# Kernel optimization log

Hardware: AMD Instinct MI355X
Metric: run time of the kernel (lower is better)

Reference implementation:

```python
import math
import jax, jax.numpy as jnp
import numpy as np

EPS = 1e-5
D_MODEL, N_HEADS, D_HEAD = 512, 8, 64


def make_signed_quant(num_bits):
    Qn = -2 ** (num_bits - 1)
    Qp = 2 ** (num_bits - 1) - 1

    @jax.custom_vjp
    def quant(x, alpha):
        a = jnp.maximum(alpha, EPS)
        return jnp.clip(jnp.round(x / a), Qn, Qp) * a

    def fwd(x, alpha):
        a = jnp.maximum(alpha, EPS)
        return jnp.clip(jnp.round(x / a), Qn, Qp) * a, (x, a)

    def bwd(res, g):
        x, a = res
        qw = x / a
        small = (qw < Qn).astype(g.dtype)
        big = (qw > Qp).astype(g.dtype)
        mid = 1.0 - small - big
        gs = 1.0 / math.sqrt(x.size * Qp)
        ga = jnp.sum((small * Qn + big * Qp + mid * (jnp.round(qw) - qw)) * g) * gs
        return mid * g, ga.reshape(())

    quant.defvjp(fwd, bwd)
    return quant


def make_unsigned_quant(num_bits):
    Qp = 2 ** num_bits - 1

    @jax.custom_vjp
    def quant(x, alpha):
        a = jnp.maximum(alpha, EPS)
        mn = jnp.min(x)
        return jnp.clip(jnp.round((x - mn) / a), 0, Qp) * a + mn

    def fwd(x, alpha):
        a = jnp.maximum(alpha, EPS)
        mn = jnp.min(x)
        return jnp.clip(jnp.round((x - mn) / a), 0, Qp) * a + mn, (x - mn, a)

    def bwd(res, g):
        xs, a = res
        qw = xs / a
        small = (qw < 0).astype(g.dtype)
        big = (qw > Qp).astype(g.dtype)
        mid = 1.0 - small - big
        gs = 1.0 / math.sqrt(xs.size * Qp)
        ga = jnp.sum((big * Qp + mid * (jnp.round(qw) - qw)) * g) * gs
        return mid * g, ga.reshape(())

    quant.defvjp(fwd, bwd)
    return quant


def _bwn_body(w):
    # layerwise BWN: sign(w - mean(w)) * mean(|w|)
    m = jnp.mean(jnp.abs(w))
    e = jnp.mean(w)
    return jnp.sign(w - e) * m


@jax.custom_vjp
def bwn(w):
    return _bwn_body(w)


def _bwn_fwd(w):
    return _bwn_body(w), None


def _bwn_bwd(_, g):
    return (g,)  # straight-through


bwn.defvjp(_bwn_fwd, _bwn_bwd)

sig4 = make_signed_quant(4)
sig8 = make_signed_quant(8)  # the output QuantizeLinear uses default input_bits=8
uns4 = make_unsigned_quant(4)


def layernorm(x, g, b):
    mu = jnp.mean(x, axis=-1, keepdims=True)
    var = jnp.var(x, axis=-1, keepdims=True)
    return (x - mu) / jnp.sqrt(var + 1e-5) * g + b


def attention_forward(q, k, v, Wq, Wk, Wv, Wo, bq, bk, bv, ln_g, ln_b,
                      aq_in, ak_in, av_in, a_cq, a_ck, a_cv, a_cattn, ao_in):
    B, S, _ = q.shape
    # QuantizeLinear: 4-bit elastic act quant + BWN binary weights, NO bias; then LearnableBias add
    Q = sig4(q, aq_in) @ bwn(Wq).T + bq
    K = sig4(k, ak_in) @ bwn(Wk).T + bk
    V = sig4(v, av_in) @ bwn(Wv).T + bv

    def split(x):  # [B,S,H*d] -> [B,H,S,d]
        return jnp.transpose(x.reshape(B, -1, N_HEADS, D_HEAD), (0, 2, 1, 3))

    Q, K, V = split(Q), split(K), split(V)
    Q = sig4(Q, a_cq)
    K = sig4(K, a_ck)
    V = sig4(V, a_cv)
    scores = jnp.einsum('bhqd,bhkd->bhqk', Q, K) / math.sqrt(D_HEAD)
    # NOTE: original calls scores.masked_fill(mask==0, -1e9) WITHOUT assignment,
    # so the mask has no effect on the math; replicated faithfully.
    attn = jax.nn.softmax(scores, axis=-1)
    attn = uns4(attn, a_cattn)
    ctx = jnp.einsum('bhqk,bhkd->bhqd', attn, V)
    # faithful to original `.view(B, S, H*d)` on the [B,H,S,d] tensor (no head transpose)
    ctx = ctx.reshape(B, S, N_HEADS * D_HEAD)
    out = sig8(ctx, ao_in) @ bwn(Wo).T
    return layernorm(q + out, ln_g, ln_b), scores


def setup_inputs() -> dict:
    key = jax.random.key(0)
    ks = jax.random.split(key, 8)
    B, S, D = 4, 1024, 512
    f = jnp.float32
    return {
        'q': jax.random.normal(ks[0], (B, S, D), f),
        'k': jax.random.normal(ks[1], (B, S, D), f),
        'v': jax.random.normal(ks[2], (B, S, D), f),
        'mask': jnp.ones((B, 1, S, S), jnp.int32),
        'Wq': jax.random.normal(ks[3], (D, D), f) * 0.02,
        'Wk': jax.random.normal(ks[4], (D, D), f) * 0.02,
        'Wv': jax.random.normal(ks[5], (D, D), f) * 0.02,
        'Wo': jax.random.normal(ks[6], (D, D), f) * 0.02,
        'bq': jnp.zeros((D,), f),
        'bk': jnp.zeros((D,), f),
        'bv': jnp.zeros((D,), f),
        'ln_g': jnp.ones((D,), f),
        'ln_b': jnp.zeros((D,), f),
        'aq_in': jnp.asarray(0.5, f),
        'ak_in': jnp.asarray(0.5, f),
        'av_in': jnp.asarray(0.5, f),
        'a_cq': jnp.asarray(0.2, f),
        'a_ck': jnp.asarray(0.2, f),
        'a_cv': jnp.asarray(0.2, f),
        'a_cattn': jnp.asarray(0.002, f),
        'ao_in': jnp.asarray(0.01, f),
    }


def reference(q, k, v, mask, Wq, Wk, Wv, Wo, bq, bk, bv, ln_g, ln_b,
              aq_in, ak_in, av_in, a_cq, a_ck, a_cv, a_cattn, ao_in):
    # mask is structurally unused (original masked_fill is not in-place and discarded)
    return attention_forward(q, k, v, Wq, Wk, Wv, Wo, bq, bk, bv, ln_g, ln_b,
                             aq_in, ak_in, av_in, a_cq, a_ck, a_cv, a_cattn, ao_in)
```

## Files before the change

kernel.cpp:

```cpp
#include <hip/hip_runtime.h>
#include <math.h>
#include <stdint.h>

#define EPSQ 1e-5f
#define WELEM 262144
#define OUT0N 2097152

#define O_WSUM   0
#define O_WABS   16
#define O_MN     32
#define O_COLSUM 64
#define O_SIGNS  16384
#define O_KQ     (O_SIGNS + 4*WELEM)
#define O_KK     (O_KQ + 2097152)
#define O_KV     (O_KK + 2097152)
#define O_VT     (O_KV + 2097152)
#define O_RMAX   (O_VT + 2097152)
#define O_RSUM   (O_RMAX + 131072)
#define O_CTXQ   (O_RSUM + 131072)
#define O_OUTB   (O_CTXQ + 2097152)
#define O_RCAND  O_OUTB

#define AS 72

typedef __bf16 bf16x8 __attribute__((ext_vector_type(8)));
typedef __bf16 bf16x4 __attribute__((ext_vector_type(4)));
typedef float  floatx4 __attribute__((ext_vector_type(4)));

__device__ __forceinline__ float clampf(float x, float lo, float hi) {
  return fminf(fmaxf(x, lo), hi);
}

__device__ __forceinline__ void unpack16(__bf16* dst, int4 raw) {
  const int8_t* sb = (const int8_t*)&raw;
  __bf16 tmp[16];
#pragma unroll
  for (int j = 0; j < 16; ++j) tmp[j] = (__bf16)(float)sb[j];
  *(bf16x8*)&dst[0] = *(bf16x8*)&tmp[0];
  *(bf16x8*)&dst[8] = *(bf16x8*)&tmp[8];
}

__global__ void k_init(float* wsum, float* wabs) {
  int t = threadIdx.x;
  if (t < 4) { wsum[t] = 0.f; wabs[t] = 0.f; }
}

__global__ void k_wstats(const float* Wq, const float* Wk, const float* Wv, const float* Wo,
                         float* wsum, float* wabs) {
  __shared__ float s1[256], s2[256];
  int w = blockIdx.x >> 6;
  const float* W = (w == 0) ? Wq : (w == 1) ? Wk : (w == 2) ? Wv : Wo;
  int base = (blockIdx.x & 63) * 4096;
  float s = 0.f, sa = 0.f;
  for (int i = threadIdx.x; i < 4096; i += 256) {
    float x = W[base + i];
    s += x; sa += fabsf(x);
  }
  s1[threadIdx.x] = s; s2[threadIdx.x] = sa; __syncthreads();
  for (int o = 128; o > 0; o >>= 1) {
    if (threadIdx.x < o) { s1[threadIdx.x] += s1[threadIdx.x + o]; s2[threadIdx.x] += s2[threadIdx.x + o]; }
    __syncthreads();
  }
  if (threadIdx.x == 0) { atomicAdd(&wsum[w], s1[0]); atomicAdd(&wabs[w], s2[0]); }
}

__global__ void k_sign(const float* Wq, const float* Wk, const float* Wv, const float* Wo,
                       const float* wsum, int8_t* signs) {
  int idx = blockIdx.x * 256 + threadIdx.x;
  int w = idx >> 18;
  int pos = idx & (WELEM - 1);
  const float* W = (w == 0) ? Wq : (w == 1) ? Wk : (w == 2) ? Wv : Wo;
  float e = wsum[w] * (1.0f / 262144.0f);
  float x = W[pos];
  signs[idx] = (int8_t)((x > e) - (x < e));
}

__global__ __launch_bounds__(256) void k_proj(
    const float* q, const float* kin, const float* vin,
    const float* bq, const float* bk, const float* bv,
    const float* aq, const float* ak, const float* av,
    const float* acq, const float* ack, const float* acv,
    const int8_t* signs, const float* wabs,
    int8_t* kqo, int8_t* kko, int8_t* kvo) {
  __shared__ __align__(16) __bf16 As[64][AS];
  __shared__ __align__(16) __bf16 Bs[64][AS];
  int z = blockIdx.z;
  const float* X    = (z == 0) ? q   : (z == 1) ? kin : vin;
  const float* bias = (z == 0) ? bq  : (z == 1) ? bk  : bv;
  const float* aip  = (z == 0) ? aq  : (z == 1) ? ak  : av;
  const float* ahp  = (z == 0) ? acq : (z == 1) ? ack : acv;
  int8_t* outp      = (z == 0) ? kqo : (z == 1) ? kko : kvo;
  float a_in = fmaxf(aip[0], EPSQ);
  float a_hd = fmaxf(ahp[0], EPSQ);
  float m_w  = wabs[z] * (1.0f / 262144.0f);
  const int8_t* S = signs + (size_t)z * WELEM;

  int n0 = blockIdx.x * 64;
  int f0 = blockIdx.y * 64;
  int t = threadIdx.x;
  int lane = t & 63, w = t >> 6, quad = lane >> 4, l16 = lane & 15;
  int c4 = (t & 15) * 4, mb = t >> 4;
  int k16 = (t & 3) * 16, mrow = t >> 2;
  floatx4 acc[4];
#pragma unroll
  for (int nt = 0; nt < 4; ++nt) acc[nt] = (floatx4){0.f, 0.f, 0.f, 0.f};

  for (int k0 = 0; k0 < 512; k0 += 64) {
#pragma unroll
    for (int j = 0; j < 4; ++j) {
      int m = mb + j * 16;
      float4 x = *(const float4*)&X[(size_t)(n0 + m) * 512 + k0 + c4];
      bf16x4 av = { (__bf16)clampf(rintf(x.x / a_in), -8.f, 7.f),
                    (__bf16)clampf(rintf(x.y / a_in), -8.f, 7.f),
                    (__bf16)clampf(rintf(x.z / a_in), -8.f, 7.f),
                    (__bf16)clampf(rintf(x.w / a_in), -8.f, 7.f) };
      *(bf16x4*)&As[m][c4] = av;
    }
    {
      int4 raw = *(const int4*)&S[(size_t)(f0 + mrow) * 512 + k0 + k16];
      unpack16(&Bs[mrow][k16], raw);
    }
    __syncthreads();
#pragma unroll
    for (int kh = 0; kh < 64; kh += 32) {
      bf16x8 a = *(const bf16x8*)&As[w * 16 + l16][kh + quad * 8];
#pragma unroll
      for (int nt = 0; nt < 4; ++nt) {
        bf16x8 b = *(const bf16x8*)&Bs[nt * 16 + l16][kh + quad * 8];
        acc[nt] = __builtin_amdgcn_mfma_f32_16x16x32_bf16(a, b, acc[nt], 0, 0, 0);
      }
    }
    __syncthreads();
  }
  float s_am = a_in * m_w;
#pragma unroll
  for (int nt = 0; nt < 4; ++nt) {
    int f = f0 + nt * 16 + l16;
    int h = f >> 6, dd = f & 63;
    float bia = bias[f];
#pragma unroll
    for (int r = 0; r < 4; ++r) {
      int n = n0 + w * 16 + quad * 4 + r;
      int b = n >> 10, srow = n & 1023;
      float P = s_am * acc[nt][r] + bia;
      float hq = clampf(rintf(P / a_hd), -8.f, 7.f);
      outp[(size_t)((b * 8 + h) * 1024 + srow) * 64 + dd] = (int8_t)hq;
    }
  }
}

__global__ __launch_bounds__(256) void k_vt(const int8_t* kv, int8_t* vt, int* colsum) {
  __shared__ int red[256];
  int bh = blockIdx.x;
  int t = threadIdx.x;
  int dd = t & 63, part = t >> 6;
  const int8_t* p = kv + (size_t)bh * 65536;
  int8_t* o = vt + (size_t)bh * 65536;
  int acc = 0;
  for (int s = part * 256; s < part * 256 + 256; ++s) {
    int8_t val = p[s * 64 + dd];
    o[dd * 1024 + s] = val;
    acc += val;
  }
  red[t] = acc; __syncthreads();
  if (part == 0) colsum[bh * 64 + dd] = red[dd] + red[64 + dd] + red[128 + dd] + red[192 + dd];
}

__global__ __launch_bounds__(256) void k_qks(
    const int8_t* kq, const int8_t* kkv,
    const float* acq, const float* ack,
    float* scores, float* rmax, float* rsum, float* rcand) {
  __shared__ __align__(16) __bf16 As[64][AS];
  __shared__ __align__(16) __bf16 Bs[64][AS];
  int bh = blockIdx.y;
  int q0 = blockIdx.x * 64;
  const int8_t* A  = kq  + (size_t)bh * 65536;
  const int8_t* Bp = kkv + (size_t)bh * 65536;
  float* Sp = scores + ((size_t)bh * 1024 + q0) * 1024;
  int t = threadIdx.x;
  int lane = t & 63, w = t >> 6, quad = lane >> 4, l16 = lane & 15;
  int k16 = (t & 3) * 16, mrow = t >> 2;
  float sc = fmaxf(acq[0], EPSQ) * fmaxf(ack[0], EPSQ) * 0.125f;

  {
    int4 ra = *(const int4*)&A[(q0 + mrow) * 64 + k16];
    unpack16(&As[mrow][k16], ra);
  }
  float m_run[4], l_run[4], mn_run[4];
#pragma unroll
  for (int rr = 0; rr < 4; ++rr) { m_run[rr] = -INFINITY; l_run[rr] = 0.f; mn_run[rr] = INFINITY; }

  for (int ct = 0; ct < 16; ++ct) {
    __syncthreads();
    {
      int4 rb = *(const int4*)&Bp[(ct * 64 + mrow) * 64 + k16];
      unpack16(&Bs[mrow][k16], rb);
    }
    __syncthreads();
    floatx4 acc[4];
#pragma unroll
    for (int nt = 0; nt < 4; ++nt) acc[nt] = (floatx4){0.f, 0.f, 0.f, 0.f};
#pragma unroll
    for (int kh = 0; kh < 64; kh += 32) {
      bf16x8 a = *(const bf16x8*)&As[w * 16 + l16][kh + quad * 8];
#pragma unroll
      for (int nt = 0; nt < 4; ++nt) {
        bf16x8 b = *(const bf16x8*)&Bs[nt * 16 + l16][kh + quad * 8];
        acc[nt] = __builtin_amdgcn_mfma_f32_16x16x32_bf16(a, b, acc[nt], 0, 0, 0);
      }
    }
#pragma unroll
    for (int rr = 0; rr < 4; ++rr) {
      int row = w * 16 + quad * 4 + rr;
      float v[4];
#pragma unroll
      for (int nt = 0; nt < 4; ++nt) {
        v[nt] = sc * acc[nt][rr];
        Sp[(size_t)row * 1024 + ct * 64 + nt * 16 + l16] = v[nt];
      }
      float tmax = fmaxf(fmaxf(v[0], v[1]), fmaxf(v[2], v[3]));
      float tmin = fminf(fminf(v[0], v[1]), fminf(v[2], v[3]));
      mn_run[rr] = fminf(mn_run[rr], tmin);
      float mnew = fmaxf(m_run[rr], tmax);
      float s = 0.f;
#pragma unroll
      for (int nt = 0; nt < 4; ++nt) s += expf(v[nt] - mnew);
      l_run[rr] = l_run[rr] * expf(m_run[rr] - mnew) + s;
      m_run[rr] = mnew;
    }
  }
#pragma unroll
  for (int o = 1; o < 16; o <<= 1) {
#pragma unroll
    for (int rr = 0; rr < 4; ++rr) {
      float mo = __shfl_xor(m_run[rr], o);
      float lo = __shfl_xor(l_run[rr], o);
      float mnew = fmaxf(m_run[rr], mo);
      l_run[rr] = l_run[rr] * expf(m_run[rr] - mnew) + lo * expf(mo - mnew);
      m_run[rr] = mnew;
      mn_run[rr] = fminf(mn_run[rr], __shfl_xor(mn_run[rr], o));
    }
  }
  if (l16 == 0) {
#pragma unroll
    for (int rr = 0; rr < 4; ++rr) {
      int r = bh * 1024 + q0 + w * 16 + quad * 4 + rr;
      rmax[r] = m_run[rr];
      rsum[r] = l_run[rr];
      rcand[r] = expf(mn_run[rr] - m_run[rr]) * (1.0f / l_run[rr]);
    }
  }
}

__global__ __launch_bounds__(1024) void k_minred(const float* rcand, float* mnf) {
  __shared__ float red[1024];
  float mn = INFINITY;
  for (int i = threadIdx.x; i < 32768; i += 1024) mn = fminf(mn, rcand[i]);
  red[threadIdx.x] = mn; __syncthreads();
  for (int o = 512; o > 0; o >>= 1) {
    if (threadIdx.x < o) red[threadIdx.x] = fminf(red[threadIdx.x], red[threadIdx.x + o]);
    __syncthreads();
  }
  if (threadIdx.x == 0) mnf[0] = red[0];
}

__global__ __launch_bounds__(256) void k_pv(
    const float* scores, const float* rmax, const float* rsum,
    const float* mnf, const int* colsum, const int8_t* vt,
    const float* acattn, const float* acv, const float* ao,
    int8_t* ctxq) {
  __shared__ __align__(16) __bf16 As[32][AS];
  __shared__ __align__(16) __bf16 Bs[64][AS];
  int bh = blockIdx.y;
  int m0 = blockIdx.x * 32;
  float mn = mnf[0];
  float a_att = fmaxf(acattn[0], EPSQ);
  float a_v   = fmaxf(acv[0], EPSQ);
  float a_o   = fmaxf(ao[0], EPSQ);
  const float* Sp  = scores + (size_t)bh * 1048576;
  const int8_t* Vt = vt + (size_t)bh * 65536;
  int t = threadIdx.x;
  int lane = t & 63, w = t >> 6, quad = lane >> 4, l16 = lane & 15;
  int mt = w & 1, np = w >> 1;
  int c4 = (t & 15) * 4, mb = t >> 4;
  int k16 = (t & 3) * 16, mrow = t >> 2;
  float rm[2], rs[2];
#pragma unroll
  for (int j = 0; j < 2; ++j) {
    int r = bh * 1024 + m0 + mb + j * 16;
    rm[j] = rmax[r]; rs[j] = rsum[r];
  }
  floatx4 acc[2];
  acc[0] = (floatx4){0.f, 0.f, 0.f, 0.f};
  acc[1] = (floatx4){0.f, 0.f, 0.f, 0.f};

  for (int k0 = 0; k0 < 1024; k0 += 64) {
#pragma unroll
    for (int j = 0; j < 2; ++j) {
      int m = mb + j * 16;
      float4 s4 = *(const float4*)&Sp[(size_t)(m0 + m) * 1024 + k0 + c4];
      float inv = 1.0f / rs[j];
      bf16x4 av = {
        (__bf16)clampf(rintf((expf(s4.x - rm[j]) * inv - mn) / a_att), 0.f, 15.f),
        (__bf16)clampf(rintf((expf(s4.y - rm[j]) * inv - mn) / a_att), 0.f, 15.f),
        (__bf16)clampf(rintf((expf(s4.z - rm[j]) * inv - mn) / a_att), 0.f, 15.f),
        (__bf16)clampf(rintf((expf(s4.w - rm[j]) * inv - mn) / a_att), 0.f, 15.f) };
      *(bf16x4*)&As[m][c4] = av;
    }
    {
      int4 raw = *(const int4*)&Vt[(size_t)mrow * 1024 + k0 + k16];
      unpack16(&Bs[mrow][k16], raw);
    }
    __syncthreads();
#pragma unroll
    for (int kh = 0; kh < 64; kh += 32) {
      bf16x8 a = *(const bf16x8*)&As[mt * 16 + l16][kh + quad * 8];
#pragma unroll
      for (int j = 0; j < 2; ++j) {
        bf16x8 b = *(const bf16x8*)&Bs[(np * 2 + j) * 16 + l16][kh + quad * 8];
        acc[j] = __builtin_amdgcn_mfma_f32_16x16x32_bf16(a, b, acc[j], 0, 0, 0);
      }
    }
    __syncthreads();
  }
  float sc  = a_att * a_v;
  float mnv = mn * a_v;
  int b = bh >> 3, h = bh & 7;
#pragma unroll
  for (int j = 0; j < 2; ++j) {
    int dd = (np * 2 + j) * 16 + l16;
    float cs = (float)colsum[bh * 64 + dd];
#pragma unroll
    for (int r = 0; r < 4; ++r) {
      int srow = m0 + mt * 16 + quad * 4 + r;
      float ctx = sc * acc[j][r] + mnv * cs;
      float c8 = clampf(rintf(ctx / a_o), -128.f, 127.f);
      ctxq[(size_t)b * 524288 + (size_t)(h * 128 + (srow >> 3)) * 512 + (srow & 7) * 64 + dd] = (int8_t)c8;
    }
  }
}

__global__ __launch_bounds__(256) void k_outg(
    const int8_t* ctxq, const int8_t* signs_o,
    const float* wabs, const float* ao, float* outb) {
  __shared__ __align__(16) __bf16 As[64][AS];
  __shared__ __align__(16) __bf16 Bs[64][AS];
  int n0 = blockIdx.x * 64, f0 = blockIdx.y * 64;
  int t = threadIdx.x;
  int lane = t & 63, w = t >> 6, quad = lane >> 4, l16 = lane & 15;
  int k16 = (t & 3) * 16, mrow = t >> 2;
  floatx4 acc[4];
#pragma unroll
  for (int nt = 0; nt < 4; ++nt) acc[nt] = (floatx4){0.f, 0.f, 0.f, 0.f};
  for (int k0 = 0; k0 < 512; k0 += 64) {
    {
      int4 ra = *(const int4*)&ctxq[(size_t)(n0 + mrow) * 512 + k0 + k16];
      int4 rb = *(const int4*)&signs_o[(size_t)(f0 + mrow) * 512 + k0 + k16];
      unpack16(&As[mrow][k16], ra);
      unpack16(&Bs[mrow][k16], rb);
    }
    __syncthreads();
#pragma unroll
    for (int kh = 0; kh < 64; kh += 32) {
      bf16x8 a = *(const bf16x8*)&As[w * 16 + l16][kh + quad * 8];
#pragma unroll
      for (int nt = 0; nt < 4; ++nt) {
        bf16x8 b = *(const bf16x8*)&Bs[nt * 16 + l16][kh + quad * 8];
        acc[nt] = __builtin_amdgcn_mfma_f32_16x16x32_bf16(a, b, acc[nt], 0, 0, 0);
      }
    }
    __syncthreads();
  }
  float scale = fmaxf(ao[0], EPSQ) * (wabs[3] * (1.0f / 262144.0f));
#pragma unroll
  for (int nt = 0; nt < 4; ++nt)
#pragma unroll
    for (int r = 0; r < 4; ++r)
      outb[(size_t)(n0 + w * 16 + quad * 4 + r) * 512 + f0 + nt * 16 + l16] = scale * acc[nt][r];
}

__global__ __launch_bounds__(256) void k_ln(
    const float* q, const float* outb, const float* g, const float* bb, float* out0) {
  __shared__ float red[256];
  int r = blockIdx.x, t = threadIdx.x;
  const float* qp = q + (size_t)r * 512;
  const float* op = outb + (size_t)r * 512;
  float y0 = qp[t] + op[t];
  float y1 = qp[t + 256] + op[t + 256];
  red[t] = y0 + y1; __syncthreads();
  for (int o = 128; o > 0; o >>= 1) { if (t < o) red[t] += red[t + o]; __syncthreads(); }
  float mu = red[0] * (1.0f / 512.0f); __syncthreads();
  float d0 = y0 - mu, d1 = y1 - mu;
  red[t] = d0 * d0 + d1 * d1; __syncthreads();
  for (int o = 128; o > 0; o >>= 1) { if (t < o) red[t] += red[t + o]; __syncthreads(); }
  float var = red[0] * (1.0f / 512.0f);
  float den = sqrtf(var + 1e-5f);
  out0[(size_t)r * 512 + t]       = d0 / den * g[t] + bb[t];
  out0[(size_t)r * 512 + t + 256] = d1 / den * g[t + 256] + bb[t + 256];
}

extern "C" void kernel_launch(void* const* d_in, const int* in_sizes, int n_in,
                              void* d_out, int out_size, void* d_ws, size_t ws_size,
                              hipStream_t stream) {
  const float* q   = (const float*)d_in[0];
  const float* k   = (const float*)d_in[1];
  const float* v   = (const float*)d_in[2];
  const float* Wq  = (const float*)d_in[4];
  const float* Wk  = (const float*)d_in[5];
  const float* Wv  = (const float*)d_in[6];
  const float* Wo  = (const float*)d_in[7];
  const float* bq  = (const float*)d_in[8];
  const float* bk  = (const float*)d_in[9];
  const float* bv  = (const float*)d_in[10];
  const float* lng = (const float*)d_in[11];
  const float* lnb = (const float*)d_in[12];
  const float* aq  = (const float*)d_in[13];
  const float* ak  = (const float*)d_in[14];
  const float* av  = (const float*)d_in[15];
  const float* acq = (const float*)d_in[16];
  const float* ack = (const float*)d_in[17];
  const float* acv = (const float*)d_in[18];
  const float* aca = (const float*)d_in[19];
  const float* ao  = (const float*)d_in[20];

  char* ws = (char*)d_ws;
  float* wsum   = (float*)(ws + O_WSUM);
  float* wabs   = (float*)(ws + O_WABS);
  float* mnf    = (float*)(ws + O_MN);
  int*   colsum = (int*)(ws + O_COLSUM);
  int8_t* signs = (int8_t*)(ws + O_SIGNS);
  int8_t* kqb   = (int8_t*)(ws + O_KQ);
  int8_t* kkb   = (int8_t*)(ws + O_KK);
  int8_t* kvb   = (int8_t*)(ws + O_KV);
  int8_t* vtb   = (int8_t*)(ws + O_VT);
  float* rmax   = (float*)(ws + O_RMAX);
  float* rsum   = (float*)(ws + O_RSUM);
  float* rcand  = (float*)(ws + O_RCAND);
  int8_t* ctxq  = (int8_t*)(ws + O_CTXQ);
  float* outb   = (float*)(ws + O_OUTB);

  float* out0   = (float*)d_out;
  float* scores = (float*)d_out + OUT0N;

  k_init<<<1, 64, 0, stream>>>(wsum, wabs);
  k_wstats<<<256, 256, 0, stream>>>(Wq, Wk, Wv, Wo, wsum, wabs);
  k_sign<<<4096, 256, 0, stream>>>(Wq, Wk, Wv, Wo, wsum, signs);
  k_proj<<<dim3(64, 8, 3), 256, 0, stream>>>(q, k, v, bq, bk, bv, aq, ak, av,
                                             acq, ack, acv, signs, wabs, kqb, kkb, kvb);
  k_vt<<<32, 256, 0, stream>>>(kvb, vtb, colsum);
  k_qks<<<dim3(16, 32), 256, 0, stream>>>(kqb, kkb, acq, ack, scores, rmax, rsum, rcand);
  k_minred<<<1, 1024, 0, stream>>>(rcand, mnf);
  k_pv<<<dim3(32, 32), 256, 0, stream>>>(scores, rmax, rsum, mnf, colsum, vtb,
                                         aca, acv, ao, ctxq);
  k_outg<<<dim3(64, 8), 256, 0, stream>>>(ctxq, signs + 3 * WELEM, wabs, ao, outb);
  k_ln<<<4096, 256, 0, stream>>>(q, outb, lng, lnb, out0);
}
```

Before: 417.0 us.

## Store quantized intermediates as bf16 and fuse V transpose into projection

Intermediate quantized tensors (weight signs, Q/K heads, transposed V, context) are now stored directly as bf16 instead of int8, so the GEMM tile loaders copy without int8-to-bf16 unpacking. The separate k_vt transpose/colsum kernel is removed: the projection kernel writes V transposed and accumulates column sums with float atomics. This doubles intermediate memory traffic and adds atomic contention, in exchange for one fewer launch and a poorly parallel (32-block) kernel disappearing.

```diff
diff --git a/kernel.cpp b/kernel.cpp
--- a/kernel.cpp
+++ b/kernel.cpp
@@ -10,15 +10,14 @@
 #define O_WABS   16
 #define O_MN     32
 #define O_COLSUM 64
-#define O_SIGNS  16384
-#define O_KQ     (O_SIGNS + 4*WELEM)
-#define O_KK     (O_KQ + 2097152)
-#define O_KV     (O_KK + 2097152)
-#define O_VT     (O_KV + 2097152)
-#define O_RMAX   (O_VT + 2097152)
+#define O_WSIGNS 16384
+#define O_KQ     (O_WSIGNS + 8*WELEM)
+#define O_CTXQ   O_KQ
+#define O_KK     (O_KQ + 4194304)
+#define O_VT     (O_KK + 4194304)
+#define O_RMAX   (O_VT + 4194304)
 #define O_RSUM   (O_RMAX + 131072)
-#define O_CTXQ   (O_RSUM + 131072)
-#define O_OUTB   (O_CTXQ + 2097152)
+#define O_OUTB   (O_RSUM + 131072)
 #define O_RCAND  O_OUTB
 
 #define AS 72
@@ -31,18 +30,10 @@
   return fminf(fmaxf(x, lo), hi);
 }
 
-__device__ __forceinline__ void unpack16(__bf16* dst, int4 raw) {
-  const int8_t* sb = (const int8_t*)&raw;
-  __bf16 tmp[16];
-#pragma unroll
-  for (int j = 0; j < 16; ++j) tmp[j] = (__bf16)(float)sb[j];
-  *(bf16x8*)&dst[0] = *(bf16x8*)&tmp[0];
-  *(bf16x8*)&dst[8] = *(bf16x8*)&tmp[8];
-}
-
-__global__ void k_init(float* wsum, float* wabs) {
+__global__ void k_init(float* wsum, float* wabs, float* colsum) {
   int t = threadIdx.x;
   if (t < 4) { wsum[t] = 0.f; wabs[t] = 0.f; }
+  for (int i = t; i < 2048; i += 256) colsum[i] = 0.f;
 }
 
 __global__ void k_wstats(const float* Wq, const float* Wk, const float* Wv, const float* Wo,
@@ -65,14 +56,14 @@
 }
 
 __global__ void k_sign(const float* Wq, const float* Wk, const float* Wv, const float* Wo,
-                       const float* wsum, int8_t* signs) {
+                       const float* wsum, __bf16* wsigns) {
   int idx = blockIdx.x * 256 + threadIdx.x;
   int w = idx >> 18;
   int pos = idx & (WELEM - 1);
   const float* W = (w == 0) ? Wq : (w == 1) ? Wk : (w == 2) ? Wv : Wo;
   float e = wsum[w] * (1.0f / 262144.0f);
   float x = W[pos];
-  signs[idx] = (int8_t)((x > e) - (x < e));
+  wsigns[idx] = (__bf16)(float)((x > e) - (x < e));
 }
 
 __global__ __launch_bounds__(256) void k_proj(
@@ -80,8 +71,8 @@
     const float* bq, const float* bk, const float* bv,
     const float* aq, const float* ak, const float* av,
     const float* acq, const float* ack, const float* acv,
-    const int8_t* signs, const float* wabs,
-    int8_t* kqo, int8_t* kko, int8_t* kvo) {
+    const __bf16* wsigns, const float* wabs,
+    __bf16* kqo, __bf16* kko, __bf16* vto, float* colsum) {
   __shared__ __align__(16) __bf16 As[64][AS];
   __shared__ __align__(16) __bf16 Bs[64][AS];
   int z = blockIdx.z;
@@ -89,18 +80,17 @@
   const float* bias = (z == 0) ? bq  : (z == 1) ? bk  : bv;
   const float* aip  = (z == 0) ? aq  : (z == 1) ? ak  : av;
   const float* ahp  = (z == 0) ? acq : (z == 1) ? ack : acv;
-  int8_t* outp      = (z == 0) ? kqo : (z == 1) ? kko : kvo;
   float a_in = fmaxf(aip[0], EPSQ);
   float a_hd = fmaxf(ahp[0], EPSQ);
   float m_w  = wabs[z] * (1.0f / 262144.0f);
-  const int8_t* S = signs + (size_t)z * WELEM;
+  const __bf16* S = wsigns + (size_t)z * WELEM;
 
   int n0 = blockIdx.x * 64;
   int f0 = blockIdx.y * 64;
   int t = threadIdx.x;
   int lane = t & 63, w = t >> 6, quad = lane >> 4, l16 = lane & 15;
   int c4 = (t & 15) * 4, mb = t >> 4;
-  int k16 = (t & 3) * 16, mrow = t >> 2;
+  int e16 = (t & 3) * 16, mrow = t >> 2;
   floatx4 acc[4];
 #pragma unroll
   for (int nt = 0; nt < 4; ++nt) acc[nt] = (floatx4){0.f, 0.f, 0.f, 0.f};
@@ -117,8 +107,9 @@
       *(bf16x4*)&As[m][c4] = av;
     }
     {
-      int4 raw = *(const int4*)&S[(size_t)(f0 + mrow) * 512 + k0 + k16];
-      unpack16(&Bs[mrow][k16], raw);
+      const __bf16* src = &S[(size_t)(f0 + mrow) * 512 + k0 + e16];
+      *(bf16x8*)&Bs[mrow][e16]     = *(const bf16x8*)src;
+      *(bf16x8*)&Bs[mrow][e16 + 8] = *(const bf16x8*)(src + 8);
     }
     __syncthreads();
 #pragma unroll
@@ -133,58 +124,66 @@
     __syncthreads();
   }
   float s_am = a_in * m_w;
-#pragma unroll
-  for (int nt = 0; nt < 4; ++nt) {
-    int f = f0 + nt * 16 + l16;
-    int h = f >> 6, dd = f & 63;
-    float bia = bias[f];
-#pragma unroll
-    for (int r = 0; r < 4; ++r) {
-      int n = n0 + w * 16 + quad * 4 + r;
-      int b = n >> 10, srow = n & 1023;
-      float P = s_am * acc[nt][r] + bia;
-      float hq = clampf(rintf(P / a_hd), -8.f, 7.f);
-      outp[(size_t)((b * 8 + h) * 1024 + srow) * 64 + dd] = (int8_t)hq;
-    }
-  }
-}
-
-__global__ __launch_bounds__(256) void k_vt(const int8_t* kv, int8_t* vt, int* colsum) {
-  __shared__ int red[256];
-  int bh = blockIdx.x;
-  int t = threadIdx.x;
-  int dd = t & 63, part = t >> 6;
-  const int8_t* p = kv + (size_t)bh * 65536;
-  int8_t* o = vt + (size_t)bh * 65536;
-  int acc = 0;
-  for (int s = part * 256; s < part * 256 + 256; ++s) {
-    int8_t val = p[s * 64 + dd];
-    o[dd * 1024 + s] = val;
-    acc += val;
-  }
-  red[t] = acc; __syncthreads();
-  if (part == 0) colsum[bh * 64 + dd] = red[dd] + red[64 + dd] + red[128 + dd] + red[192 + dd];
+  if (z != 2) {
+    __bf16* outp = (z == 0) ? kqo : kko;
+#pragma unroll
+    for (int nt = 0; nt < 4; ++nt) {
+      int f = f0 + nt * 16 + l16;
+      int h = f >> 6, dd = f & 63;
+      float bia = bias[f];
+#pragma unroll
+      for (int r = 0; r < 4; ++r) {
+        int n = n0 + w * 16 + quad * 4 + r;
+        int b = n >> 10, srow = n & 1023;
+        float P = s_am * acc[nt][r] + bia;
+        float hq = clampf(rintf(P / a_hd), -8.f, 7.f);
+        outp[(size_t)((b * 8 + h) * 1024 + srow) * 64 + dd] = (__bf16)hq;
+      }
+    }
+  } else {
+    int b = n0 >> 10;
+    int srow0 = (n0 & 1023) + w * 16 + quad * 4;
+#pragma unroll
+    for (int nt = 0; nt < 4; ++nt) {
+      int f = f0 + nt * 16 + l16;
+      int h = f >> 6, dd = f & 63;
+      int bh = b * 8 + h;
+      float bia = bias[f];
+      float part = 0.f;
+      bf16x4 pack;
+#pragma unroll
+      for (int r = 0; r < 4; ++r) {
+        float P = s_am * acc[nt][r] + bia;
+        float hq = clampf(rintf(P / a_hd), -8.f, 7.f);
+        pack[r] = (__bf16)hq;
+        part += hq;
+      }
+      *(bf16x4*)&vto[((size_t)bh * 64 + dd) * 1024 + srow0] = pack;
+      atomicAdd(&colsum[bh * 64 + dd], part);
+    }
+  }
 }
 
 __global__ __launch_bounds__(256) void k_qks(
-    const int8_t* kq, const int8_t* kkv,
+    const __bf16* kq, const __bf16* kkv,
     const float* acq, const float* ack,
     float* scores, float* rmax, float* rsum, float* rcand) {
   __shared__ __align__(16) __bf16 As[64][AS];
   __shared__ __align__(16) __bf16 Bs[64][AS];
   int bh = blockIdx.y;
   int q0 = blockIdx.x * 64;
-  const int8_t* A  = kq  + (size_t)bh * 65536;
-  const int8_t* Bp = kkv + (size_t)bh * 65536;
+  const __bf16* A  = kq  + (size_t)bh * 65536;
+  const __bf16* Bp = kkv + (size_t)bh * 65536;
   float* Sp = scores + ((size_t)bh * 1024 + q0) * 1024;
   int t = threadIdx.x;
   int lane = t & 63, w = t >> 6, quad = lane >> 4, l16 = lane & 15;
-  int k16 = (t & 3) * 16, mrow = t >> 2;
+  int e16 = (t & 3) * 16, mrow = t >> 2;
   float sc = fmaxf(acq[0], EPSQ) * fmaxf(ack[0], EPSQ) * 0.125f;
 
   {
-    int4 ra = *(const int4*)&A[(q0 + mrow) * 64 + k16];
-    unpack16(&As[mrow][k16], ra);
+    const __bf16* src = &A[(q0 + mrow) * 64 + e16];
+    *(bf16x8*)&As[mrow][e16]     = *(const bf16x8*)src;
+    *(bf16x8*)&As[mrow][e16 + 8] = *(const bf16x8*)(src + 8);
   }
   float m_run[4], l_run[4], mn_run[4];
 #pragma unroll
@@ -193,8 +192,9 @@
   for (int ct = 0; ct < 16; ++ct) {
     __syncthreads();
     {
-      int4 rb = *(const int4*)&Bp[(ct * 64 + mrow) * 64 + k16];
-      unpack16(&Bs[mrow][k16], rb);
+      const __bf16* src = &Bp[(ct * 64 + mrow) * 64 + e16];
+      *(bf16x8*)&Bs[mrow][e16]     = *(const bf16x8*)src;
+      *(bf16x8*)&Bs[mrow][e16 + 8] = *(const bf16x8*)(src + 8);
     }
     __syncthreads();
     floatx4 acc[4];
@@ -266,9 +266,9 @@
 
 __global__ __launch_bounds__(256) void k_pv(
     const float* scores, const float* rmax, const float* rsum,
-    const float* mnf, const int* colsum, const int8_t* vt,
+    const float* mnf, const float* colsum, const __bf16* vt,
     const float* acattn, const float* acv, const float* ao,
-    int8_t* ctxq) {
+    __bf16* ctxq) {
   __shared__ __align__(16) __bf16 As[32][AS];
   __shared__ __align__(16) __bf16 Bs[64][AS];
   int bh = blockIdx.y;
@@ -278,12 +278,12 @@
   float a_v   = fmaxf(acv[0], EPSQ);
   float a_o   = fmaxf(ao[0], EPSQ);
   const float* Sp  = scores + (size_t)bh * 1048576;
-  const int8_t* Vt = vt + (size_t)bh * 65536;
+  const __bf16* Vt = vt + (size_t)bh * 65536;
   int t = threadIdx.x;
   int lane = t & 63, w = t >> 6, quad = lane >> 4, l16 = lane & 15;
   int mt = w & 1, np = w >> 1;
   int c4 = (t & 15) * 4, mb = t >> 4;
-  int k16 = (t & 3) * 16, mrow = t >> 2;
+  int e16 = (t & 3) * 16, mrow = t >> 2;
   float rm[2], rs[2];
 #pragma unroll
   for (int j = 0; j < 2; ++j) {
@@ -308,8 +308,9 @@
       *(bf16x4*)&As[m][c4] = av;
     }
     {
-      int4 raw = *(const int4*)&Vt[(size_t)mrow * 1024 + k0 + k16];
-      unpack16(&Bs[mrow][k16], raw);
+      const __bf16* src = &Vt[(size_t)mrow * 1024 + k0 + e16];
+      *(bf16x8*)&Bs[mrow][e16]     = *(const bf16x8*)src;
+      *(bf16x8*)&Bs[mrow][e16 + 8] = *(const bf16x8*)(src + 8);
     }
     __syncthreads();
 #pragma unroll
@@ -329,35 +330,37 @@
 #pragma unroll
   for (int j = 0; j < 2; ++j) {
     int dd = (np * 2 + j) * 16 + l16;
-    float cs = (float)colsum[bh * 64 + dd];
+    float cs = colsum[bh * 64 + dd];
 #pragma unroll
     for (int r = 0; r < 4; ++r) {
       int srow = m0 + mt * 16 + quad * 4 + r;
       float ctx = sc * acc[j][r] + mnv * cs;
       float c8 = clampf(rintf(ctx / a_o), -128.f, 127.f);
-      ctxq[(size_t)b * 524288 + (size_t)(h * 128 + (srow >> 3)) * 512 + (srow & 7) * 64 + dd] = (int8_t)c8;
+      ctxq[(size_t)b * 524288 + (size_t)(h * 128 + (srow >> 3)) * 512 + (srow & 7) * 64 + dd] = (__bf16)c8;
     }
   }
 }
 
 __global__ __launch_bounds__(256) void k_outg(
-    const int8_t* ctxq, const int8_t* signs_o,
+    const __bf16* ctxq, const __bf16* signs_o,
     const float* wabs, const float* ao, float* outb) {
   __shared__ __align__(16) __bf16 As[64][AS];
   __shared__ __align__(16) __bf16 Bs[64][AS];
   int n0 = blockIdx.x * 64, f0 = blockIdx.y * 64;
   int t = threadIdx.x;
   int lane = t & 63, w = t >> 6, quad = lane >> 4, l16 = lane & 15;
-  int k16 = (t & 3) * 16, mrow = t >> 2;
+  int e16 = (t & 3) * 16, mrow = t >> 2;
   floatx4 acc[4];
 #pragma unroll
   for (int nt = 0; nt < 4; ++nt) acc[nt] = (floatx4){0.f, 0.f, 0.f, 0.f};
   for (int k0 = 0; k0 < 512; k0 += 64) {
     {
-      int4 ra = *(const int4*)&ctxq[(size_t)(n0 + mrow) * 512 + k0 + k16];
-      int4 rb = *(const int4*)&signs_o[(size_t)(f0 + mrow) * 512 + k0 + k16];
-      unpack16(&As[mrow][k16], ra);
-      unpack16(&Bs[mrow][k16], rb);
+      const __bf16* sa = &ctxq[(size_t)(n0 + mrow) * 512 + k0 + e16];
+      const __bf16* sb = &signs_o[(size_t)(f0 + mrow) * 512 + k0 + e16];
+      *(bf16x8*)&As[mrow][e16]     = *(const bf16x8*)sa;
+      *(bf16x8*)&As[mrow][e16 + 8] = *(const bf16x8*)(sa + 8);
+      *(bf16x8*)&Bs[mrow][e16]     = *(const bf16x8*)sb;
+      *(bf16x8*)&Bs[mrow][e16 + 8] = *(const bf16x8*)(sb + 8);
     }
     __syncthreads();
 #pragma unroll
@@ -424,34 +427,33 @@
   const float* ao  = (const float*)d_in[20];
 
   char* ws = (char*)d_ws;
-  float* wsum   = (float*)(ws + O_WSUM);
-  float* wabs   = (float*)(ws + O_WABS);
-  float* mnf    = (float*)(ws + O_MN);
-  int*   colsum = (int*)(ws + O_COLSUM);
-  int8_t* signs = (int8_t*)(ws + O_SIGNS);
-  int8_t* kqb   = (int8_t*)(ws + O_KQ);
-  int8_t* kkb   = (int8_t*)(ws + O_KK);
-  int8_t* kvb   = (int8_t*)(ws + O_KV);
-  int8_t* vtb   = (int8_t*)(ws + O_VT);
-  float* rmax   = (float*)(ws + O_RMAX);
-  float* rsum   = (float*)(ws + O_RSUM);
-  float* rcand  = (float*)(ws + O_RCAND);
-  int8_t* ctxq  = (int8_t*)(ws + O_CTXQ);
-  float* outb   = (float*)(ws + O_OUTB);
+  float*  wsum   = (float*)(ws + O_WSUM);
+  float*  wabs   = (float*)(ws + O_WABS);
+  float*  mnf    = (float*)(ws + O_MN);
+  float*  colsum = (float*)(ws + O_COLSUM);
+  __bf16* wsigns = (__bf16*)(ws + O_WSIGNS);
+  __bf16* kqb    = (__bf16*)(ws + O_KQ);
+  __bf16* kkb    = (__bf16*)(ws + O_KK);
+  __bf16* vtb    = (__bf16*)(ws + O_VT);
+  float*  rmax   = (float*)(ws + O_RMAX);
+  float*  rsum   = (float*)(ws + O_RSUM);
+  float*  rcand  = (float*)(ws + O_RCAND);
+  __bf16* ctxq   = (__bf16*)(ws + O_CTXQ);
+  float*  outb   = (float*)(ws + O_OUTB);
 
   float* out0   = (float*)d_out;
   float* scores = (float*)d_out + OUT0N;
 
-  k_init<<<1, 64, 0, stream>>>(wsum, wabs);
+  k_init<<<1, 256, 0, stream>>>(wsum, wabs, colsum);
   k_wstats<<<256, 256, 0, stream>>>(Wq, Wk, Wv, Wo, wsum, wabs);
-  k_sign<<<4096, 256, 0, stream>>>(Wq, Wk, Wv, Wo, wsum, signs);
+  k_sign<<<4096, 256, 0, stream>>>(Wq, Wk, Wv, Wo, wsum, wsigns);
   k_proj<<<dim3(64, 8, 3), 256, 0, stream>>>(q, k, v, bq, bk, bv, aq, ak, av,
-                                             acq, ack, acv, signs, wabs, kqb, kkb, kvb);
-  k_vt<<<32, 256, 0, stream>>>(kvb, vtb, colsum);
+                                             acq, ack, acv, wsigns, wabs,
+                                             kqb, kkb, vtb, colsum);
   k_qks<<<dim3(16, 32), 256, 0, stream>>>(kqb, kkb, acq, ack, scores, rmax, rsum, rcand);
   k_minred<<<1, 1024, 0, stream>>>(rcand, mnf);
   k_pv<<<dim3(32, 32), 256, 0, stream>>>(scores, rmax, rsum, mnf, colsum, vtb,
                                          aca, acv, ao, ctxq);
-  k_outg<<<dim3(64, 8), 256, 0, stream>>>(ctxq, signs + 3 * WELEM, wabs, ao, outb);
+  k_outg<<<dim3(64, 8), 256, 0, stream>>>(ctxq, wsigns + 3 * WELEM, wabs, ao, outb);
   k_ln<<<4096, 256, 0, stream>>>(q, outb, lng, lnb, out0);
 }
```

Result: faster. 378.5 us (-9.2%).
